# Optimization experiments

Measured on AMD Instinct MI355X. Metric: run time of the kernel, lower is better.

## Reference

```python
import jax, jax.numpy as jnp
import numpy as np
from jax import lax

KS = 3
PAD = 1
N = KS * KS


def setup_inputs() -> dict:
    key = jax.random.key(0)
    k1, k2, k3, k4, k5, k6 = jax.random.split(key, 6)
    b, cin, cout, h, w = 4, 64, 64, 256, 256
    x = jax.random.normal(k1, (b, cin, h, w), jnp.float32)
    # offset-predicting conv: 2*N output channels, 3x3, pad 1
    p_conv_w = 0.1 * jax.random.normal(k2, (2 * N, cin, KS, KS), jnp.float32)
    p_conv_b = jnp.zeros((2 * N,), jnp.float32)
    # main conv applied to the k*k-expanded sampled map (no bias in original)
    conv_w = jax.random.normal(k3, (cout, cin, KS, KS), jnp.float32) / np.sqrt(cin * N)
    bn_gamma = 1.0 + 0.1 * jax.random.normal(k4, (cout,), jnp.float32)
    bn_beta = 0.1 * jax.random.normal(k5, (cout,), jnp.float32)
    return {"x": x, "p_conv_w": p_conv_w, "p_conv_b": p_conv_b,
            "conv_w": conv_w, "bn_gamma": bn_gamma, "bn_beta": bn_beta}


def _deform_conv(x, p_conv_w, p_conv_b, conv_w, bn_gamma, bn_beta):
    b, c, h, w = x.shape
    # offsets: (b, 2N, h, w) -> (b, h, w, 2N)
    offset = lax.conv_general_dilated(x, p_conv_w, (1, 1), ((PAD, PAD), (PAD, PAD)))
    offset = offset + p_conv_b[None, :, None, None]
    offset = jnp.transpose(offset, (0, 2, 3, 1))
    # zero-pad input; sampling coordinates live on the padded grid
    x_pad = jnp.pad(x, ((0, 0), (0, 0), (PAD, PAD), (PAD, PAD)))
    Hp, Wp = h + 2 * PAD, w + 2 * PAD
    # p = p_0 + p_n + offset  (x/y coords each of shape (b,h,w,N))
    r = jnp.arange(-(KS - 1) // 2, KS // 2 + 1, dtype=jnp.float32)  # [-1,0,1]
    pn_x, pn_y = jnp.meshgrid(r, r, indexing="ij")
    pn_x, pn_y = pn_x.reshape(-1), pn_y.reshape(-1)  # (N,)
    p0_x = jnp.arange(1, h + 1, dtype=jnp.float32)[:, None, None]  # (h,1,1)
    p0_y = jnp.arange(1, w + 1, dtype=jnp.float32)[None, :, None]  # (1,w,1)
    p_x = offset[..., :N] + p0_x + pn_x  # (b,h,w,N)
    p_y = offset[..., N:] + p0_y + pn_y
    # integer corner coords (detached / non-differentiable), clamped
    fx = jnp.floor(lax.stop_gradient(p_x))
    fy = jnp.floor(lax.stop_gradient(p_y))
    q_lt_x = jnp.clip(fx, 0, Hp - 1).astype(jnp.int32)
    q_lt_y = jnp.clip(fy, 0, Wp - 1).astype(jnp.int32)
    q_rb_x = jnp.clip(fx + 1, 0, Hp - 1).astype(jnp.int32)
    q_rb_y = jnp.clip(fy + 1, 0, Wp - 1).astype(jnp.int32)
    # clamped continuous coords (gradient flows to offsets)
    px = jnp.clip(p_x, 0, Hp - 1)
    py = jnp.clip(p_y, 0, Wp - 1)
    # bilinear weights
    ltx = q_lt_x.astype(px.dtype); lty = q_lt_y.astype(px.dtype)
    rbx = q_rb_x.astype(px.dtype); rby = q_rb_y.astype(px.dtype)
    g_lt = (1 + (ltx - px)) * (1 + (lty - py))
    g_rb = (1 - (rbx - px)) * (1 - (rby - py))
    g_lb = (1 + (ltx - px)) * (1 - (rby - py))
    g_rt = (1 - (rbx - px)) * (1 + (lty - py))
    x_flat = x_pad.reshape(b, c, Hp * Wp)

    def gather(qx, qy):
        idx = (qx * Wp + qy).reshape(b, 1, -1)  # (b,1,h*w*N)
        out = jnp.take_along_axis(x_flat, idx, axis=2)
        return out.reshape(b, c, h, w, N)

    x_off = (g_lt[:, None] * gather(q_lt_x, q_lt_y)
             + g_rb[:, None] * gather(q_rb_x, q_rb_y)
             + g_lb[:, None] * gather(q_lt_x, q_rb_y)
             + g_rt[:, None] * gather(q_rb_x, q_lt_y))  # (b,c,h,w,N)
    # conv (kernel=KS, stride=KS on k*k-expanded map) == contraction over (c,N)
    out = jnp.einsum("bchwn,ocn->bohw", x_off, conv_w.reshape(conv_w.shape[0], c, N))
    # BatchNorm2d (training-mode batch statistics) + LeakyReLU(0.1)
    mean = out.mean(axis=(0, 2, 3), keepdims=True)
    var = out.var(axis=(0, 2, 3), keepdims=True)
    y = (out - mean) * lax.rsqrt(var + 1e-5)
    y = y * bn_gamma[None, :, None, None] + bn_beta[None, :, None, None]
    return jnp.where(y > 0, y, 0.1 * y)


def reference(x, p_conv_w, p_conv_b, conv_w, bn_gamma, bn_beta):
    return _deform_conv(x, p_conv_w, p_conv_b, conv_w, bn_gamma, bn_beta)
```

## Files before the change

kernel.cpp:

```cpp
#include <hip/hip_runtime.h>
#include <math.h>

#define BB 4
#define CC 64
#define OCC 64
#define HH 256
#define WW 256
#define HP 258
#define WP 258
#define NPIX (BB * HH * WW)
#define CNT_F 262144.0f

typedef __attribute__((ext_vector_type(8))) __bf16 bf16x8;
typedef __attribute__((ext_vector_type(4))) float f32x4;

__device__ __forceinline__ float blo(unsigned u) {
    return __builtin_bit_cast(float, u << 16);
}
__device__ __forceinline__ float bhi(unsigned u) {
    return __builtin_bit_cast(float, u & 0xffff0000u);
}

__global__ __launch_bounds__(256) void pad_transpose(const float* __restrict__ x,
                                                     __bf16* __restrict__ xt) {
    int blk = blockIdx.x;
    int xchunk = blk & 3;
    int y = (blk >> 2) & 255;
    int b = blk >> 10;
    int tid = threadIdx.x;
    __shared__ float tile[64][65];
    int x0 = xchunk * 64;
    int col = tid & 63;
    int crow = tid >> 6;
    const float* xp = x + ((size_t)b * CC) * HH * WW + (size_t)y * WW + x0;
#pragma unroll
    for (int i = 0; i < 16; ++i) {
        int c = crow + i * 4;
        tile[c][col] = xp[(size_t)c * HH * WW + col];
    }
    __syncthreads();
    __bf16* op = xt + (((size_t)b * HP + (y + 1)) * WP + (x0 + 1)) * CC;
#pragma unroll
    for (int i = 0; i < 16; ++i) {
        int xl = crow + i * 4;
        op[(size_t)xl * CC + col] = (__bf16)tile[col][xl];
    }
}

__global__ void zero_border(__bf16* __restrict__ xt) {
    int i = blockIdx.x * 256 + threadIdx.x;
    const int total = BB * 1028 * CC;
    if (i >= total) return;
    int c = i & 63;
    int p = (i >> 6) % 1028;
    int b = (i >> 6) / 1028;
    int yp, xp;
    if (p < 258)      { yp = 0;           xp = p; }
    else if (p < 516) { yp = 257;         xp = p - 258; }
    else if (p < 772) { yp = p - 516 + 1; xp = 0; }
    else              { yp = p - 772 + 1; xp = 257; }
    xt[(((size_t)b * HP + yp) * WP + xp) * CC + c] = (__bf16)0.0f;
}

__global__ void reorder_weights(const float* __restrict__ cw,
                                const float* __restrict__ pw,
                                __bf16* __restrict__ wtb,
                                __bf16* __restrict__ pwb) {
    int i = blockIdx.x * 256 + threadIdx.x;
    if (i < 36864) {
        int c = i & 63;
        int n = (i >> 6) % 9;
        int oc = i / 576;
        wtb[i] = (__bf16)cw[((size_t)oc * CC + c) * 9 + n];
    } else {
        int j = i - 36864;
        if (j >= 18432) return;
        int c = j & 63;
        int n = (j >> 6) % 9;
        int oc = j / 576;
        pwb[j] = (__bf16)(oc < 18 ? pw[((size_t)oc * CC + c) * 9 + n] : 0.0f);
    }
}

__global__ __launch_bounds__(256, 8) void offset_strip(const __bf16* __restrict__ xt,
                                                       const __bf16* __restrict__ pwb,
                                                       const float* __restrict__ pb,
                                                       float* __restrict__ off) {
    int phys = blockIdx.x;
    int blk = (phys & 7) * 1024 + (phys >> 3);
    int xq = blk & 7;
    int y  = (blk >> 3) & 255;
    int b  = blk >> 11;
    int x0 = xq * 32;
    int tid = threadIdx.x;
    int wave = tid >> 6, lane = tid & 63;

    __shared__ __attribute__((aligned(16))) __bf16 sS[3][34][72];

    {
        const char* base = (const char*)xt + (size_t)b * HP * WP * CC * 2;
        for (int t = tid; t < 3264; t += 256) {
            int pos = t >> 5, cp = t & 31;
            int r = pos / 34, j = pos - r * 34;
            unsigned d = *(const unsigned*)(base
                + (size_t)((y + r) * WP + (x0 + j)) * (CC * 2) + cp * 4);
            *(unsigned*)&sS[r][j][cp * 2] = d;
        }
    }
    __syncthreads();

    int mh = wave & 1, nh = wave >> 1;
    int m = lane & 15, q = lane >> 4;
    int p_a = mh * 16 + m;
    f32x4 acc = {0.0f, 0.0f, 0.0f, 0.0f};
    const __bf16* bp = pwb + (size_t)(nh * 16 + m) * 576 + q * 8;
#pragma unroll
    for (int n = 0; n < 9; ++n) {
        int dy = n / 3, dx = n - dy * 3;
        const __bf16* abase = &sS[dy][p_a + dx][q * 8];
#pragma unroll
        for (int h = 0; h < 2; ++h) {
            bf16x8 a  = *(const bf16x8*)(abase + h * 32);
            bf16x8 bv = *(const bf16x8*)(bp + n * 64 + h * 32);
            acc = __builtin_amdgcn_mfma_f32_16x16x32_bf16(a, bv, acc, 0, 0, 0);
        }
    }
    int oc = nh * 16 + m;
    if (oc < 18) {
        float bias = pb[oc];
        float* ob = off + (((size_t)(b * 18 + oc)) * HH + y) * WW + x0 + mh * 16 + q * 4;
        float4 v;
        v.x = acc[0] + bias;
        v.y = acc[1] + bias;
        v.z = acc[2] + bias;
        v.w = acc[3] + bias;
        *(float4*)ob = v;
    }
}

__global__ __launch_bounds__(256, 6) void deform_mfma16(const __bf16* __restrict__ xt,
                                                        const float* __restrict__ off,
                                                        const __bf16* __restrict__ wtb,
                                                        float* __restrict__ out) {
    int phys = blockIdx.x;
    int blk = (phys & 7) * 2048 + (phys >> 3);
    int xh = blk & 15;
    int y  = (blk >> 4) & 255;
    int b  = blk >> 12;
    int x0 = xh * 16;
    int tid = threadIdx.x;
    int wave = tid >> 6, lane = tid & 63;
    int chp = lane & 31, half = lane >> 5;

    __shared__ __attribute__((aligned(16))) __bf16 sA[16][584];
    __shared__ __attribute__((aligned(16))) float scratch[1152];
    float* cg = scratch;
    int*   cb = (int*)(scratch + 576);

    if (tid < 144) {
        int t = tid;
        int n = t >> 4, p = t & 15;
        float offx = off[(((size_t)(b * 18 + n)) * HH + y) * WW + x0 + p];
        float offy = off[(((size_t)(b * 18 + n + 9)) * HH + y) * WW + x0 + p];
        float px = offx + (float)(y + 1) + (float)(n / 3 - 1);
        float py = offy + (float)(x0 + p + 1) + (float)(n % 3 - 1);
        float fx = floorf(px), fy = floorf(py);
        float pxc = fminf(fmaxf(px, 0.0f), 257.0f);
        float pyc = fminf(fmaxf(py, 0.0f), 257.0f);
        int ltx = (int)fminf(fmaxf(fx, 0.0f), 257.0f);
        int lty = (int)fminf(fmaxf(fy, 0.0f), 257.0f);
        int rbx = (int)fminf(fmaxf(fx + 1.0f, 0.0f), 257.0f);
        int rby = (int)fminf(fmaxf(fy + 1.0f, 0.0f), 257.0f);
        float dxl = 1.0f + ((float)ltx - pxc);
        float dxr = 1.0f - ((float)rbx - pxc);
        float dyl = 1.0f + ((float)lty - pyc);
        float dyr = 1.0f - ((float)rby - pyc);
        cg[t * 4 + 0] = dxl * dyl;
        cg[t * 4 + 1] = dxr * dyr;
        cg[t * 4 + 2] = dxl * dyr;
        cg[t * 4 + 3] = dxr * dyl;
        cb[t * 4 + 0] = ((ltx * WP + lty) * CC) * 2;
        cb[t * 4 + 1] = ((rbx * WP + rby) * CC) * 2;
        cb[t * 4 + 2] = ((ltx * WP + rby) * CC) * 2;
        cb[t * 4 + 3] = ((rbx * WP + lty) * CC) * 2;
    }
    __syncthreads();

    {
        const char* xbl = (const char*)xt + (size_t)b * HP * WP * CC * 2 + (size_t)chp * 4;
        const float4* cg4 = (const float4*)scratch;
        const int4*   cb4 = (const int4*)(scratch + 576);
#pragma unroll 6
        for (int r = 0; r < 18; ++r) {
            int t = wave * 36 + r * 2 + half;
            float4 g = cg4[t];
            int4 cv = cb4[t];
            unsigned d0 = *(const unsigned*)(xbl + cv.x);
            unsigned d1 = *(const unsigned*)(xbl + cv.y);
            unsigned d2 = *(const unsigned*)(xbl + cv.z);
            unsigned d3 = *(const unsigned*)(xbl + cv.w);
            float lo = g.x * blo(d0) + g.y * blo(d1) + g.z * blo(d2) + g.w * blo(d3);
            float hi = g.x * bhi(d0) + g.y * bhi(d1) + g.z * bhi(d2) + g.w * bhi(d3);
            __bf16 rlo = (__bf16)lo, rhi = (__bf16)hi;
            ushort2 rv;
            rv.x = __builtin_bit_cast(unsigned short, rlo);
            rv.y = __builtin_bit_cast(unsigned short, rhi);
            int n = t >> 4, p = t & 15;
            *(ushort2*)&sA[p][n * 64 + chp * 2] = rv;
        }
    }
    __syncthreads();

    int m = lane & 15, q = lane >> 4;
    f32x4 acc = {0.0f, 0.0f, 0.0f, 0.0f};
    {
        const __bf16* arow = &sA[m][q * 8];
        const __bf16* bp = wtb + (size_t)(wave * 16 + m) * 576 + q * 8;
#pragma unroll
        for (int k0 = 0; k0 < 576; k0 += 32) {
            bf16x8 a  = *(const bf16x8*)(arow + k0);
            bf16x8 bv = *(const bf16x8*)(bp + k0);
            acc = __builtin_amdgcn_mfma_f32_16x16x32_bf16(a, bv, acc, 0, 0, 0);
        }
    }

    int oc = wave * 16 + m;
    float* ob = out + (((size_t)b * OCC + oc) * HH + y) * WW + x0 + q * 4;
    float4 v;
    v.x = acc[0]; v.y = acc[1]; v.z = acc[2]; v.w = acc[3];
    *(float4*)ob = v;
}

__global__ __launch_bounds__(256) void stats_kernel(const float* __restrict__ out,
                                                    float* __restrict__ stats) {
    int blk = blockIdx.x;
    int b = blk & 3;
    int oc = blk >> 2;
    const float* p = out + ((size_t)b * OCC + oc) * HH * WW;
    float s = 0.0f, q = 0.0f;
    for (int i = threadIdx.x; i < HH * WW; i += 256) {
        float v = p[i];
        s += v;
        q += v * v;
    }
#pragma unroll
    for (int d = 1; d < 64; d <<= 1) {
        s += __shfl_xor(s, d, 64);
        q += __shfl_xor(q, d, 64);
    }
    __shared__ float sm[8];
    int wave = threadIdx.x >> 6, lane = threadIdx.x & 63;
    if (lane == 0) { sm[wave] = s; sm[4 + wave] = q; }
    __syncthreads();
    if (threadIdx.x == 0) {
        float ts = sm[0] + sm[1] + sm[2] + sm[3];
        float tq = sm[4] + sm[5] + sm[6] + sm[7];
        atomicAdd(&stats[oc], ts);
        atomicAdd(&stats[64 + oc], tq);
    }
}

__global__ __launch_bounds__(256) void bn_leaky(float* __restrict__ out,
                                                const float* __restrict__ stats,
                                                const float* __restrict__ gamma,
                                                const float* __restrict__ beta) {
    int i = blockIdx.x * 256 + threadIdx.x;
    int oc = (i >> 14) & 63;
    float mean = stats[oc] * (1.0f / CNT_F);
    float var = stats[64 + oc] * (1.0f / CNT_F) - mean * mean;
    float scale = gamma[oc] * rsqrtf(var + 1e-5f);
    float shift = beta[oc] - mean * scale;
    float4* o4 = (float4*)out;
    float4 v = o4[i];
    v.x = v.x * scale + shift; v.x = v.x > 0.0f ? v.x : 0.1f * v.x;
    v.y = v.y * scale + shift; v.y = v.y > 0.0f ? v.y : 0.1f * v.y;
    v.z = v.z * scale + shift; v.z = v.z > 0.0f ? v.z : 0.1f * v.z;
    v.w = v.w * scale + shift; v.w = v.w > 0.0f ? v.w : 0.1f * v.w;
    o4[i] = v;
}

extern "C" void kernel_launch(void* const* d_in, const int* in_sizes, int n_in,
                              void* d_out, int out_size, void* d_ws, size_t ws_size,
                              hipStream_t stream) {
    (void)in_sizes; (void)n_in; (void)out_size; (void)ws_size;
    const float* x     = (const float*)d_in[0];
    const float* pw    = (const float*)d_in[1];
    const float* pb    = (const float*)d_in[2];
    const float* cw    = (const float*)d_in[3];
    const float* gamma = (const float*)d_in[4];
    const float* beta  = (const float*)d_in[5];
    float* out = (float*)d_out;
    char* ws = (char*)d_ws;

    __bf16* xtb  = (__bf16*)ws;
    float*  off  = (float*)(ws + 34080768);
    __bf16* wtb  = (__bf16*)(ws + 34080768 + 18874368);
    __bf16* pwb  = (__bf16*)(ws + 34080768 + 18874368 + 73728);
    float*  stats = (float*)(ws + 34080768 + 18874368 + 73728 + 36864);

    hipMemsetAsync(stats, 0, 128 * sizeof(float), stream);
    pad_transpose<<<4096, 256, 0, stream>>>(x, xtb);
    zero_border<<<(BB * 1028 * CC + 255) / 256, 256, 0, stream>>>(xtb);
    reorder_weights<<<216, 256, 0, stream>>>(cw, pw, wtb, pwb);
    offset_strip<<<8192, 256, 0, stream>>>(xtb, pwb, pb, off);
    deform_mfma16<<<16384, 256, 0, stream>>>(xtb, off, wtb, out);
    stats_kernel<<<OCC * BB, 256, 0, stream>>>(out, stats);
    bn_leaky<<<NPIX * OCC / 4 / 256, 256, 0, stream>>>(out, stats, gamma, beta);
}
```

Before: 455.0 us.

## Keep sampling coefficients in registers via shuffles, swizzle LDS, raise occupancy

Each wave now computes its own 36 bilinear coefficient/offset sets in registers and broadcasts them with wave shuffles. This removes the shared scratch buffer and one block-wide barrier. The sA tile loses its padding and is accessed through an XOR swizzle to avoid bank conflicts, which cuts LDS use. Launch bounds rise to 8 blocks per CU, and s_setprio is raised around the MFMA loop. The risk is register pressure from the 8 extra live values plus the shuffle cost under the tighter occupancy target.

```diff
diff --git a/kernel.cpp b/kernel.cpp
--- a/kernel.cpp
+++ b/kernel.cpp
@@ -138,7 +138,7 @@
     }
 }
 
-__global__ __launch_bounds__(256, 6) void deform_mfma16(const __bf16* __restrict__ xt,
+__global__ __launch_bounds__(256, 8) void deform_mfma16(const __bf16* __restrict__ xt,
                                                         const float* __restrict__ off,
                                                         const __bf16* __restrict__ wtb,
                                                         float* __restrict__ out) {
@@ -152,13 +152,12 @@
     int wave = tid >> 6, lane = tid & 63;
     int chp = lane & 31, half = lane >> 5;
 
-    __shared__ __attribute__((aligned(16))) __bf16 sA[16][584];
-    __shared__ __attribute__((aligned(16))) float scratch[1152];
-    float* cg = scratch;
-    int*   cb = (int*)(scratch + 576);
-
-    if (tid < 144) {
-        int t = tid;
+    __shared__ __attribute__((aligned(16))) __bf16 sA[16][576];
+
+    float g0 = 0.0f, g1 = 0.0f, g2 = 0.0f, g3 = 0.0f;
+    int c0 = 0, c1 = 0, c2 = 0, c3 = 0;
+    if (lane < 36) {
+        int t = wave * 36 + lane;
         int n = t >> 4, p = t & 15;
         float offx = off[(((size_t)(b * 18 + n)) * HH + y) * WW + x0 + p];
         float offy = off[(((size_t)(b * 18 + n + 9)) * HH + y) * WW + x0 + p];
@@ -175,38 +174,45 @@
         float dxr = 1.0f - ((float)rbx - pxc);
         float dyl = 1.0f + ((float)lty - pyc);
         float dyr = 1.0f - ((float)rby - pyc);
-        cg[t * 4 + 0] = dxl * dyl;
-        cg[t * 4 + 1] = dxr * dyr;
-        cg[t * 4 + 2] = dxl * dyr;
-        cg[t * 4 + 3] = dxr * dyl;
-        cb[t * 4 + 0] = ((ltx * WP + lty) * CC) * 2;
-        cb[t * 4 + 1] = ((rbx * WP + rby) * CC) * 2;
-        cb[t * 4 + 2] = ((ltx * WP + rby) * CC) * 2;
-        cb[t * 4 + 3] = ((rbx * WP + lty) * CC) * 2;
-    }
-    __syncthreads();
+        g0 = dxl * dyl;
+        g1 = dxr * dyr;
+        g2 = dxl * dyr;
+        g3 = dxr * dyl;
+        c0 = ((ltx * WP + lty) * CC) * 2;
+        c1 = ((rbx * WP + rby) * CC) * 2;
+        c2 = ((ltx * WP + rby) * CC) * 2;
+        c3 = ((rbx * WP + lty) * CC) * 2;
+    }
 
     {
         const char* xbl = (const char*)xt + (size_t)b * HP * WP * CC * 2 + (size_t)chp * 4;
-        const float4* cg4 = (const float4*)scratch;
-        const int4*   cb4 = (const int4*)(scratch + 576);
-#pragma unroll 6
+        char* sAb = (char*)sA;
+#pragma unroll 3
         for (int r = 0; r < 18; ++r) {
-            int t = wave * 36 + r * 2 + half;
-            float4 g = cg4[t];
-            int4 cv = cb4[t];
-            unsigned d0 = *(const unsigned*)(xbl + cv.x);
-            unsigned d1 = *(const unsigned*)(xbl + cv.y);
-            unsigned d2 = *(const unsigned*)(xbl + cv.z);
-            unsigned d3 = *(const unsigned*)(xbl + cv.w);
-            float lo = g.x * blo(d0) + g.y * blo(d1) + g.z * blo(d2) + g.w * blo(d3);
-            float hi = g.x * bhi(d0) + g.y * bhi(d1) + g.z * bhi(d2) + g.w * bhi(d3);
+            int src = r * 2 + half;
+            float gx = __shfl(g0, src, 64);
+            float gy = __shfl(g1, src, 64);
+            float gz = __shfl(g2, src, 64);
+            float gw = __shfl(g3, src, 64);
+            int vx = __shfl(c0, src, 64);
+            int vy = __shfl(c1, src, 64);
+            int vz = __shfl(c2, src, 64);
+            int vw = __shfl(c3, src, 64);
+            unsigned d0 = *(const unsigned*)(xbl + vx);
+            unsigned d1 = *(const unsigned*)(xbl + vy);
+            unsigned d2 = *(const unsigned*)(xbl + vz);
+            unsigned d3 = *(const unsigned*)(xbl + vw);
+            float lo = gx * blo(d0) + gy * blo(d1) + gz * blo(d2) + gw * blo(d3);
+            float hi = gx * bhi(d0) + gy * bhi(d1) + gz * bhi(d2) + gw * bhi(d3);
             __bf16 rlo = (__bf16)lo, rhi = (__bf16)hi;
             ushort2 rv;
             rv.x = __builtin_bit_cast(unsigned short, rlo);
             rv.y = __builtin_bit_cast(unsigned short, rhi);
+            int t = wave * 36 + src;
             int n = t >> 4, p = t & 15;
-            *(ushort2*)&sA[p][n * 64 + chp * 2] = rv;
+            unsigned bo = (unsigned)p * 1152u + (unsigned)n * 128u + (unsigned)chp * 4u;
+            bo ^= (unsigned)((p & 7) << 4);
+            *(ushort2*)(sAb + bo) = rv;
         }
     }
     __syncthreads();
@@ -214,14 +220,19 @@
     int m = lane & 15, q = lane >> 4;
     f32x4 acc = {0.0f, 0.0f, 0.0f, 0.0f};
     {
-        const __bf16* arow = &sA[m][q * 8];
+        const char* sAb = (const char*)sA;
+        unsigned rowb = (unsigned)m * 1152u;
+        unsigned key = (unsigned)((m & 7) << 4);
         const __bf16* bp = wtb + (size_t)(wave * 16 + m) * 576 + q * 8;
+        __builtin_amdgcn_s_setprio(1);
 #pragma unroll
         for (int k0 = 0; k0 < 576; k0 += 32) {
-            bf16x8 a  = *(const bf16x8*)(arow + k0);
+            unsigned bo = rowb + (((unsigned)(k0 * 2 + q * 16)) ^ key);
+            bf16x8 a  = *(const bf16x8*)(sAb + bo);
             bf16x8 bv = *(const bf16x8*)(bp + k0);
             acc = __builtin_amdgcn_mfma_f32_16x16x32_bf16(a, bv, acc, 0, 0, 0);
         }
+        __builtin_amdgcn_s_setprio(0);
     }
 
     int oc = wave * 16 + m;
```

After: 451.7 us. About the same (-0.7%).
